# Optimization experiments

Hardware: AMD Instinct MI355X
Metric: run time of the kernel (lower is better)

## Reference

```python
import jax, jax.numpy as jnp
import numpy as np
from jax import lax

SEQ_LEN, N_FEAT, N_EMB, N_ENC, BATCH = 100, 18, 16, 16, 16384


def lstm(x, W_ih, W_hh, b_ih, b_hh, hidden):
    """PyTorch-convention LSTM (gates i,f,g,o), batch_first x: [B,T,I].
    Returns (h_seq [B,T,H], h_last [B,H])."""
    B = x.shape[0]
    # Precompute input projections for all timesteps: [B,T,4H]
    xg = jnp.einsum('bti,gi->btg', x, W_ih) + b_ih + b_hh
    W_hh_T = W_hh.T  # [H,4H]

    def step(carry, xg_t):
        h, c = carry
        g = xg_t + h @ W_hh_T                       # [B,4H]
        i, f, gg, o = jnp.split(g, 4, axis=-1)
        i = jax.nn.sigmoid(i)
        f = jax.nn.sigmoid(f)
        gg = jnp.tanh(gg)
        o = jax.nn.sigmoid(o)
        c = f * c + i * gg
        h = o * jnp.tanh(c)
        return (h, c), h

    h0 = jnp.zeros((B, hidden), x.dtype)
    c0 = jnp.zeros((B, hidden), x.dtype)
    (h_last, _), h_seq = lax.scan(step, (h0, c0), jnp.swapaxes(xg, 0, 1))
    return jnp.swapaxes(h_seq, 0, 1), h_last


def setup_inputs() -> dict:
    key = jax.random.key(0)
    ks = jax.random.split(key, 9)
    s1 = 1.0 / np.sqrt(N_EMB)
    s2 = 1.0 / np.sqrt(N_ENC)
    u = lambda k, shape, s: jax.random.uniform(k, shape, jnp.float32, -s, s)
    return {
        'x': jax.random.normal(ks[0], (BATCH, SEQ_LEN, N_FEAT), jnp.float32),
        'W_ih1': u(ks[1], (4 * N_EMB, N_FEAT), s1),
        'W_hh1': u(ks[2], (4 * N_EMB, N_EMB), s1),
        'b_ih1': u(ks[3], (4 * N_EMB,), s1),
        'b_hh1': u(ks[4], (4 * N_EMB,), s1),
        'W_ih2': u(ks[5], (4 * N_ENC, N_EMB), s2),
        'W_hh2': u(ks[6], (4 * N_ENC, N_ENC), s2),
        'b_ih2': u(ks[7], (4 * N_ENC,), s2),
        'b_hh2': u(ks[8], (4 * N_ENC,), s2),
    }


def reference(x, W_ih1, W_hh1, b_ih1, b_hh1, W_ih2, W_hh2, b_ih2, b_hh2):
    h1_seq, _ = lstm(x, W_ih1, W_hh1, b_ih1, b_hh1, N_EMB)
    h1_seq = jax.nn.relu(h1_seq)
    _, h2_last = lstm(h1_seq, W_ih2, W_hh2, b_ih2, b_hh2, N_ENC)
    return jax.nn.relu(h2_last)  # [B, N_ENC]
```

## Files before the change

### kernel.cpp

```cpp
#include <hip/hip_runtime.h>


typedef float f32x4 __attribute__((ext_vector_type(4)));
typedef __bf16 bf16x8 __attribute__((ext_vector_type(8)));
typedef unsigned int uint32x4 __attribute__((ext_vector_type(4)));

union FragU { bf16x8 v; unsigned short u[8]; unsigned int d[4]; uint32x4 q; };

#define MFMA16(A, B, C) __builtin_amdgcn_mfma_f32_16x16x32_bf16((A), (B), (C), 0, 0, 0)

static __device__ __forceinline__ unsigned short f2bf(float f) {
  unsigned int u = __builtin_bit_cast(unsigned int, f);
  u = u + 0x7FFFu + ((u >> 16) & 1u);
  return (unsigned short)(u >> 16);
}
static __device__ __forceinline__ float bfbits2f(unsigned short h) {
  unsigned int u = ((unsigned int)h) << 16;
  return __builtin_bit_cast(float, u);
}
static __device__ __forceinline__ float sigm(float x) {
  return __builtin_amdgcn_rcpf(1.0f + __builtin_amdgcn_exp2f(x * -1.4426950408889634f));
}
static __device__ __forceinline__ float tanh_(float x) {
  return 1.0f - 2.0f * __builtin_amdgcn_rcpf(1.0f + __builtin_amdgcn_exp2f(x * 2.8853900817779268f));
}
static __device__ __forceinline__ unsigned int split_pack(float v) {
  unsigned int u = __builtin_bit_cast(unsigned int, v);
  float hf = __builtin_bit_cast(float, u & 0xFFFF0000u);
  unsigned int l = __builtin_bit_cast(unsigned int, v - hf);
  return (u >> 16) | (l & 0xFFFF0000u);
}
static __device__ __forceinline__ void cvt_pair(float f0, float f1,
                                                unsigned int& hd, unsigned int& ld) {
  unsigned int u0 = __builtin_bit_cast(unsigned int, f0);
  unsigned int u1 = __builtin_bit_cast(unsigned int, f1);
  unsigned int h0 = u0 & 0xFFFF0000u;
  unsigned int h1 = u1 & 0xFFFF0000u;
  hd = (u0 >> 16) | h1;
  unsigned int l0 = __builtin_bit_cast(unsigned int, f0 - __builtin_bit_cast(float, h0));
  unsigned int l1 = __builtin_bit_cast(unsigned int, f1 - __builtin_bit_cast(float, h1));
  ld = (l0 >> 16) | (l1 & 0xFFFF0000u);
}

struct RawX { float2 a, b2, c, d; };

__global__ __launch_bounds__(256, 1) void enc_kernel(
    const float* __restrict__ x,
    const float* __restrict__ Wih1,
    const float* __restrict__ Whh1,
    const float* __restrict__ bih1,
    const float* __restrict__ bhh1,
    const float* __restrict__ Wih2,
    const float* __restrict__ Whh2,
    const float* __restrict__ bih2,
    const float* __restrict__ bhh2,
    float* __restrict__ out)
{
  const int lane = threadIdx.x & 63;
  const int b    = lane & 15;
  const int g    = lane >> 4;

  const int wid = (int)((blockIdx.x * blockDim.x + threadIdx.x) >> 6);
  const int b0  = wid * 16;

  FragU A1h[4], A1l[4], A2h[4], A2l[4], A3h[4], A3l[4], A4h[4], A4l[4];
  f32x4 bias1v[4], bias2v[4];
#pragma unroll
  for (int tn = 0; tn < 4; ++tn) {
    const int row = tn * 16 + b;
#pragma unroll
    for (int j = 0; j < 8; ++j) {
      const int k = 8 * g + j;
      if (k < 18) {
        const float w = Wih1[row * 18 + k];
        A1h[tn].u[j] = f2bf(w);
        A1l[tn].u[j] = f2bf(w - bfbits2f(A1h[tn].u[j]));
      } else {
        A1h[tn].u[j] = 0;
        A1l[tn].u[j] = 0;
      }
      const int kk = k >> 1;
      const float w2 = Whh1[row * 16 + kk];
      const float w3 = Wih2[row * 16 + kk];
      const float w4 = Whh2[row * 16 + kk];
      A2h[tn].u[j] = f2bf(w2); A2l[tn].u[j] = f2bf(w2 - bfbits2f(A2h[tn].u[j]));
      A3h[tn].u[j] = f2bf(w3); A3l[tn].u[j] = f2bf(w3 - bfbits2f(A3h[tn].u[j]));
      A4h[tn].u[j] = f2bf(w4); A4l[tn].u[j] = f2bf(w4 - bfbits2f(A4h[tn].u[j]));
    }
#pragma unroll
    for (int r = 0; r < 4; ++r) {
      const int u4 = tn * 16 + 4 * g + r;
      bias1v[tn][r] = bih1[u4] + bhh1[u4];
      bias2v[tn][r] = bih2[u4] + bhh2[u4];
    }
  }

  const float* const x0 = x + (size_t)(b0 + b) * 1800 + 8 * g;
  const int adv = (g == 3) ? 0 : 18;

  auto loadraw = [&](const float* p) -> RawX {
    RawX r;
    r.a = *(const float2*)p;
    if (g < 2) {
      r.b2 = *(const float2*)(p + 2);
      r.c  = *(const float2*)(p + 4);
      r.d  = *(const float2*)(p + 6);
    } else {
      r.b2 = r.c = r.d = make_float2(0.f, 0.f);
    }
    return r;
  };
  auto cvt = [&](const RawX& rw, FragU& hi, FragU& lo) {
    cvt_pair(rw.a.x, rw.a.y, hi.d[0], lo.d[0]);
    cvt_pair(rw.b2.x, rw.b2.y, hi.d[1], lo.d[1]);
    cvt_pair(rw.c.x, rw.c.y, hi.d[2], lo.d[2]);
    cvt_pair(rw.d.x, rw.d.y, hi.d[3], lo.d[3]);
  };

  RawX rw0 = loadraw(x0);
  RawX rw1 = loadraw(x0 + adv);
  RawX rw  = loadraw(x0 + 2 * adv);
  const float* xq = x0 + 3 * adv;

  FragU hb, h2b;
  hb.q  = (uint32x4){0u, 0u, 0u, 0u};
  h2b.q = (uint32x4){0u, 0u, 0u, 0u};
  float c1[4] = {0.f, 0.f, 0.f, 0.f};
  float c2[4] = {0.f, 0.f, 0.f, 0.f};
  float h2v[4] = {0.f, 0.f, 0.f, 0.f};

  FragU xch, xcl;
  cvt(rw0, xch, xcl);

  f32x4 ga[4];
#pragma unroll
  for (int tn = 0; tn < 4; ++tn) {
    f32x4 acc = MFMA16(A1h[tn].v, xch.v, bias1v[tn]);
    acc = MFMA16(A1l[tn].v, xch.v, acc);
    acc = MFMA16(A1h[tn].v, xcl.v, acc);
    acc = MFMA16(A2h[tn].v, hb.v, acc);
    acc = MFMA16(A2l[tn].v, hb.v, acc);
    ga[tn] = acc;
  }
  cvt(rw1, xch, xcl);

#pragma unroll 2
  for (int t = 0; t < 100; ++t) {
    FragU rb;
#pragma unroll
    for (int r = 0; r < 4; ++r) {
      const float iv = sigm(ga[0][r]);
      const float fv = sigm(ga[1][r]);
      const float gv = tanh_(ga[2][r]);
      const float ov = sigm(ga[3][r]);
      const float cc = fv * c1[r] + iv * gv;
      c1[r] = cc;
      const float h = ov * tanh_(cc);
      const unsigned int pk = split_pack(h);
      hb.d[r] = pk;
      rb.d[r] = (h > 0.f) ? pk : 0u;
    }

    f32x4 gb[4];
#pragma unroll
    for (int tn = 0; tn < 4; ++tn) {
      f32x4 acc = MFMA16(A4h[tn].v, h2b.v, bias2v[tn]);
      acc = MFMA16(A4l[tn].v, h2b.v, acc);
      acc = MFMA16(A3h[tn].v, rb.v, acc);
      acc = MFMA16(A3l[tn].v, rb.v, acc);
      gb[tn] = acc;
    }

    f32x4 gan[4];
#pragma unroll
    for (int tn = 0; tn < 4; ++tn) {
      f32x4 acc = MFMA16(A1h[tn].v, xch.v, bias1v[tn]);
      acc = MFMA16(A1l[tn].v, xch.v, acc);
      acc = MFMA16(A1h[tn].v, xcl.v, acc);
      acc = MFMA16(A2h[tn].v, hb.v, acc);
      acc = MFMA16(A2l[tn].v, hb.v, acc);
      gan[tn] = acc;
    }

    FragU nxh, nxl;
    cvt(rw, nxh, nxl);

    RawX rwn = loadraw((t <= 96) ? xq : x0);
    xq += adv;

#pragma unroll
    for (int r = 0; r < 4; ++r) {
      const float iv = sigm(gb[0][r]);
      const float fv = sigm(gb[1][r]);
      const float gv = tanh_(gb[2][r]);
      const float ov = sigm(gb[3][r]);
      const float cc = fv * c2[r] + iv * gv;
      c2[r] = cc;
      const float h = ov * tanh_(cc);
      h2v[r] = h;
      h2b.d[r] = split_pack(h);
    }

#pragma unroll
    for (int tn = 0; tn < 4; ++tn) ga[tn] = gan[tn];
    xch = nxh;
    xcl = nxl;
    rw = rwn;
  }

  f32x4 o;
#pragma unroll
  for (int r = 0; r < 4; ++r) o[r] = fmaxf(h2v[r], 0.f);
  *(f32x4*)(out + (size_t)(b0 + b) * 16 + 4 * g) = o;

  (void)x0;
}

extern "C" void kernel_launch(void* const* d_in, const int* in_sizes, int n_in,
                              void* d_out, int out_size, void* d_ws, size_t ws_size,
                              hipStream_t stream) {
  (void)in_sizes; (void)n_in; (void)d_ws; (void)ws_size; (void)out_size;
  enc_kernel<<<dim3(256), dim3(256), 0, stream>>>(
      (const float*)d_in[0],
      (const float*)d_in[1],
      (const float*)d_in[2],
      (const float*)d_in[3],
      (const float*)d_in[4],
      (const float*)d_in[5],
      (const float*)d_in[6],
      (const float*)d_in[7],
      (const float*)d_in[8],
      (float*)d_out);
}
```

Baseline: 270.3 us.

## Split the two LSTM layers into producer and consumer wavefronts linked through LDS

```diff
diff --git a/kernel.cpp b/kernel.cpp
--- a/kernel.cpp
+++ b/kernel.cpp
@@ -42,9 +42,14 @@
   ld = (l0 >> 16) | (l1 & 0xFFFF0000u);
 }
 
+static __device__ __forceinline__ void wg_barrier() {
+  asm volatile("s_waitcnt lgkmcnt(0)" ::: "memory");
+  __builtin_amdgcn_s_barrier();
+}
+
 struct RawX { float2 a, b2, c, d; };
 
-__global__ __launch_bounds__(256, 1) void enc_kernel(
+__global__ __launch_bounds__(128, 2) void enc_kernel(
     const float* __restrict__ x,
     const float* __restrict__ Wih1,
     const float* __restrict__ Whh1,
@@ -60,118 +65,74 @@
   const int b    = lane & 15;
   const int g    = lane >> 4;
 
-  const int wid = (int)((blockIdx.x * blockDim.x + threadIdx.x) >> 6);
-  const int b0  = wid * 16;
-
-  FragU A1h[4], A1l[4], A2h[4], A2l[4], A3h[4], A3l[4], A4h[4], A4l[4];
-  f32x4 bias1v[4], bias2v[4];
-#pragma unroll
-  for (int tn = 0; tn < 4; ++tn) {
-    const int row = tn * 16 + b;
-#pragma unroll
-    for (int j = 0; j < 8; ++j) {
-      const int k = 8 * g + j;
-      if (k < 18) {
-        const float w = Wih1[row * 18 + k];
-        A1h[tn].u[j] = f2bf(w);
-        A1l[tn].u[j] = f2bf(w - bfbits2f(A1h[tn].u[j]));
+  const int role = ((int)(threadIdx.x >> 6) ^ (int)blockIdx.x) & 1;
+  const int b0   = (int)blockIdx.x * 16;
+
+  __shared__ uint32x4 hxc[2][64];
+
+  if (role == 0) {
+    FragU A1h[4], A1l[4], A2h[4], A2l[4];
+    f32x4 bias1v[4];
+#pragma unroll
+    for (int tn = 0; tn < 4; ++tn) {
+      const int row = tn * 16 + b;
+#pragma unroll
+      for (int j = 0; j < 8; ++j) {
+        const int k = 8 * g + j;
+        if (k < 18) {
+          const float w = Wih1[row * 18 + k];
+          A1h[tn].u[j] = f2bf(w);
+          A1l[tn].u[j] = f2bf(w - bfbits2f(A1h[tn].u[j]));
+        } else {
+          A1h[tn].u[j] = 0;
+          A1l[tn].u[j] = 0;
+        }
+        const int kk = k >> 1;
+        const float w2 = Whh1[row * 16 + kk];
+        A2h[tn].u[j] = f2bf(w2); A2l[tn].u[j] = f2bf(w2 - bfbits2f(A2h[tn].u[j]));
+      }
+#pragma unroll
+      for (int r = 0; r < 4; ++r) {
+        const int u4 = tn * 16 + 4 * g + r;
+        bias1v[tn][r] = bih1[u4] + bhh1[u4];
+      }
+    }
+
+    const float* const x0 = x + (size_t)(b0 + b) * 1800 + 8 * g;
+    const int adv = (g == 3) ? 0 : 18;
+
+    auto loadraw = [&](const float* p) -> RawX {
+      RawX r;
+      r.a = *(const float2*)p;
+      if (g < 2) {
+        r.b2 = *(const float2*)(p + 2);
+        r.c  = *(const float2*)(p + 4);
+        r.d  = *(const float2*)(p + 6);
       } else {
-        A1h[tn].u[j] = 0;
-        A1l[tn].u[j] = 0;
-      }
-      const int kk = k >> 1;
-      const float w2 = Whh1[row * 16 + kk];
-      const float w3 = Wih2[row * 16 + kk];
-      const float w4 = Whh2[row * 16 + kk];
-      A2h[tn].u[j] = f2bf(w2); A2l[tn].u[j] = f2bf(w2 - bfbits2f(A2h[tn].u[j]));
-      A3h[tn].u[j] = f2bf(w3); A3l[tn].u[j] = f2bf(w3 - bfbits2f(A3h[tn].u[j]));
-      A4h[tn].u[j] = f2bf(w4); A4l[tn].u[j] = f2bf(w4 - bfbits2f(A4h[tn].u[j]));
-    }
-#pragma unroll
-    for (int r = 0; r < 4; ++r) {
-      const int u4 = tn * 16 + 4 * g + r;
-      bias1v[tn][r] = bih1[u4] + bhh1[u4];
-      bias2v[tn][r] = bih2[u4] + bhh2[u4];
-    }
-  }
-
-  const float* const x0 = x + (size_t)(b0 + b) * 1800 + 8 * g;
-  const int adv = (g == 3) ? 0 : 18;
-
-  auto loadraw = [&](const float* p) -> RawX {
-    RawX r;
-    r.a = *(const float2*)p;
-    if (g < 2) {
-      r.b2 = *(const float2*)(p + 2);
-      r.c  = *(const float2*)(p + 4);
-      r.d  = *(const float2*)(p + 6);
-    } else {
-      r.b2 = r.c = r.d = make_float2(0.f, 0.f);
-    }
-    return r;
-  };
-  auto cvt = [&](const RawX& rw, FragU& hi, FragU& lo) {
-    cvt_pair(rw.a.x, rw.a.y, hi.d[0], lo.d[0]);
-    cvt_pair(rw.b2.x, rw.b2.y, hi.d[1], lo.d[1]);
-    cvt_pair(rw.c.x, rw.c.y, hi.d[2], lo.d[2]);
-    cvt_pair(rw.d.x, rw.d.y, hi.d[3], lo.d[3]);
-  };
-
-  RawX rw0 = loadraw(x0);
-  RawX rw1 = loadraw(x0 + adv);
-  RawX rw  = loadraw(x0 + 2 * adv);
-  const float* xq = x0 + 3 * adv;
-
-  FragU hb, h2b;
-  hb.q  = (uint32x4){0u, 0u, 0u, 0u};
-  h2b.q = (uint32x4){0u, 0u, 0u, 0u};
-  float c1[4] = {0.f, 0.f, 0.f, 0.f};
-  float c2[4] = {0.f, 0.f, 0.f, 0.f};
-  float h2v[4] = {0.f, 0.f, 0.f, 0.f};
-
-  FragU xch, xcl;
-  cvt(rw0, xch, xcl);
-
-  f32x4 ga[4];
-#pragma unroll
-  for (int tn = 0; tn < 4; ++tn) {
-    f32x4 acc = MFMA16(A1h[tn].v, xch.v, bias1v[tn]);
-    acc = MFMA16(A1l[tn].v, xch.v, acc);
-    acc = MFMA16(A1h[tn].v, xcl.v, acc);
-    acc = MFMA16(A2h[tn].v, hb.v, acc);
-    acc = MFMA16(A2l[tn].v, hb.v, acc);
-    ga[tn] = acc;
-  }
-  cvt(rw1, xch, xcl);
-
-#pragma unroll 2
-  for (int t = 0; t < 100; ++t) {
-    FragU rb;
-#pragma unroll
-    for (int r = 0; r < 4; ++r) {
-      const float iv = sigm(ga[0][r]);
-      const float fv = sigm(ga[1][r]);
-      const float gv = tanh_(ga[2][r]);
-      const float ov = sigm(ga[3][r]);
-      const float cc = fv * c1[r] + iv * gv;
-      c1[r] = cc;
-      const float h = ov * tanh_(cc);
-      const unsigned int pk = split_pack(h);
-      hb.d[r] = pk;
-      rb.d[r] = (h > 0.f) ? pk : 0u;
-    }
-
-    f32x4 gb[4];
-#pragma unroll
-    for (int tn = 0; tn < 4; ++tn) {
-      f32x4 acc = MFMA16(A4h[tn].v, h2b.v, bias2v[tn]);
-      acc = MFMA16(A4l[tn].v, h2b.v, acc);
-      acc = MFMA16(A3h[tn].v, rb.v, acc);
-      acc = MFMA16(A3l[tn].v, rb.v, acc);
-      gb[tn] = acc;
-    }
-
-    f32x4 gan[4];
+        r.b2 = r.c = r.d = make_float2(0.f, 0.f);
+      }
+      return r;
+    };
+    auto cvt = [&](const RawX& rw_, FragU& hi, FragU& lo) {
+      cvt_pair(rw_.a.x, rw_.a.y, hi.d[0], lo.d[0]);
+      cvt_pair(rw_.b2.x, rw_.b2.y, hi.d[1], lo.d[1]);
+      cvt_pair(rw_.c.x, rw_.c.y, hi.d[2], lo.d[2]);
+      cvt_pair(rw_.d.x, rw_.d.y, hi.d[3], lo.d[3]);
+    };
+
+    RawX rw0 = loadraw(x0);
+    RawX rw1 = loadraw(x0 + adv);
+    RawX rw  = loadraw(x0 + 2 * adv);
+    const float* xq = x0 + 3 * adv;
+
+    FragU hb;
+    hb.q = (uint32x4){0u, 0u, 0u, 0u};
+    float c1[4] = {0.f, 0.f, 0.f, 0.f};
+
+    FragU xch, xcl;
+    cvt(rw0, xch, xcl);
+
+    f32x4 ga[4];
 #pragma unroll
     for (int tn = 0; tn < 4; ++tn) {
       f32x4 acc = MFMA16(A1h[tn].v, xch.v, bias1v[tn]);
@@ -179,48 +140,121 @@
       acc = MFMA16(A1h[tn].v, xcl.v, acc);
       acc = MFMA16(A2h[tn].v, hb.v, acc);
       acc = MFMA16(A2l[tn].v, hb.v, acc);
-      gan[tn] = acc;
-    }
-
-    FragU nxh, nxl;
-    cvt(rw, nxh, nxl);
-
-    RawX rwn = loadraw((t <= 96) ? xq : x0);
-    xq += adv;
-
-#pragma unroll
-    for (int r = 0; r < 4; ++r) {
-      const float iv = sigm(gb[0][r]);
-      const float fv = sigm(gb[1][r]);
-      const float gv = tanh_(gb[2][r]);
-      const float ov = sigm(gb[3][r]);
-      const float cc = fv * c2[r] + iv * gv;
-      c2[r] = cc;
-      const float h = ov * tanh_(cc);
-      h2v[r] = h;
-      h2b.d[r] = split_pack(h);
-    }
-
-#pragma unroll
-    for (int tn = 0; tn < 4; ++tn) ga[tn] = gan[tn];
-    xch = nxh;
-    xcl = nxl;
-    rw = rwn;
+      ga[tn] = acc;
+    }
+    cvt(rw1, xch, xcl);
+
+#pragma unroll 2
+    for (int t = 0; t < 100; ++t) {
+      FragU rb;
+#pragma unroll
+      for (int r = 0; r < 4; ++r) {
+        const float iv = sigm(ga[0][r]);
+        const float fv = sigm(ga[1][r]);
+        const float gv = tanh_(ga[2][r]);
+        const float ov = sigm(ga[3][r]);
+        const float cc = fv * c1[r] + iv * gv;
+        c1[r] = cc;
+        const float h = ov * tanh_(cc);
+        const unsigned int pk = split_pack(h);
+        hb.d[r] = pk;
+        rb.d[r] = (h > 0.f) ? pk : 0u;
+      }
+      hxc[t & 1][lane] = rb.q;
+
+      f32x4 gan[4];
+#pragma unroll
+      for (int tn = 0; tn < 4; ++tn) {
+        f32x4 acc = MFMA16(A1h[tn].v, xch.v, bias1v[tn]);
+        acc = MFMA16(A1l[tn].v, xch.v, acc);
+        acc = MFMA16(A1h[tn].v, xcl.v, acc);
+        acc = MFMA16(A2h[tn].v, hb.v, acc);
+        acc = MFMA16(A2l[tn].v, hb.v, acc);
+        gan[tn] = acc;
+      }
+
+      FragU nxh, nxl;
+      cvt(rw, nxh, nxl);
+      RawX rwn = loadraw((t <= 96) ? xq : x0);
+      xq += adv;
+
+#pragma unroll
+      for (int tn = 0; tn < 4; ++tn) ga[tn] = gan[tn];
+      xch = nxh;
+      xcl = nxl;
+      rw = rwn;
+
+      wg_barrier();
+    }
+  } else {
+    FragU A3h[4], A3l[4], A4h[4], A4l[4];
+    f32x4 bias2v[4];
+#pragma unroll
+    for (int tn = 0; tn < 4; ++tn) {
+      const int row = tn * 16 + b;
+#pragma unroll
+      for (int j = 0; j < 8; ++j) {
+        const int kk = (8 * g + j) >> 1;
+        const float w3 = Wih2[row * 16 + kk];
+        const float w4 = Whh2[row * 16 + kk];
+        A3h[tn].u[j] = f2bf(w3); A3l[tn].u[j] = f2bf(w3 - bfbits2f(A3h[tn].u[j]));
+        A4h[tn].u[j] = f2bf(w4); A4l[tn].u[j] = f2bf(w4 - bfbits2f(A4h[tn].u[j]));
+      }
+#pragma unroll
+      for (int r = 0; r < 4; ++r) {
+        const int u4 = tn * 16 + 4 * g + r;
+        bias2v[tn][r] = bih2[u4] + bhh2[u4];
+      }
+    }
+
+    FragU h2b;
+    h2b.q = (uint32x4){0u, 0u, 0u, 0u};
+    float c2[4] = {0.f, 0.f, 0.f, 0.f};
+    float h2v[4] = {0.f, 0.f, 0.f, 0.f};
+
+#pragma unroll 2
+    for (int t = 0; t < 100; ++t) {
+      wg_barrier();
+
+      FragU rbp;
+      rbp.q = hxc[t & 1][lane];
+
+      f32x4 gb[4];
+#pragma unroll
+      for (int tn = 0; tn < 4; ++tn) {
+        f32x4 acc = MFMA16(A4h[tn].v, h2b.v, bias2v[tn]);
+        acc = MFMA16(A4l[tn].v, h2b.v, acc);
+        acc = MFMA16(A3h[tn].v, rbp.v, acc);
+        acc = MFMA16(A3l[tn].v, rbp.v, acc);
+        gb[tn] = acc;
+      }
+
+#pragma unroll
+      for (int r = 0; r < 4; ++r) {
+        const float iv = sigm(gb[0][r]);
+        const float fv = sigm(gb[1][r]);
+        const float gv = tanh_(gb[2][r]);
+        const float ov = sigm(gb[3][r]);
+        const float cc = fv * c2[r] + iv * gv;
+        c2[r] = cc;
+        const float h = ov * tanh_(cc);
+        h2v[r] = h;
+        h2b.d[r] = split_pack(h);
+      }
+    }
+
+    f32x4 o;
+#pragma unroll
+    for (int r = 0; r < 4; ++r) o[r] = fmaxf(h2v[r], 0.f);
+    *(f32x4*)(out + (size_t)(b0 + b) * 16 + 4 * g) = o;
   }
-
-  f32x4 o;
-#pragma unroll
-  for (int r = 0; r < 4; ++r) o[r] = fmaxf(h2v[r], 0.f);
-  *(f32x4*)(out + (size_t)(b0 + b) * 16 + 4 * g) = o;
-
-  (void)x0;
 }
 
 extern "C" void kernel_launch(void* const* d_in, const int* in_sizes, int n_in,
                               void* d_out, int out_size, void* d_ws, size_t ws_size,
                               hipStream_t stream) {
   (void)in_sizes; (void)n_in; (void)d_ws; (void)ws_size; (void)out_size;
-  enc_kernel<<<dim3(256), dim3(256), 0, stream>>>(
+  enc_kernel<<<dim3(1024), dim3(128), 0, stream>>>(
       (const float*)d_in[0],
       (const float*)d_in[1],
       (const float*)d_in[2],
```

Result: no change. 275.2 us (+1.8%).

## Split input-projection MFMAs off the recurrent chain and use v_perm packing

Applied to the files above, without the earlier changes.

```diff
diff --git a/kernel.cpp b/kernel.cpp
--- a/kernel.cpp
+++ b/kernel.cpp
@@ -28,7 +28,7 @@
   unsigned int u = __builtin_bit_cast(unsigned int, v);
   float hf = __builtin_bit_cast(float, u & 0xFFFF0000u);
   unsigned int l = __builtin_bit_cast(unsigned int, v - hf);
-  return (u >> 16) | (l & 0xFFFF0000u);
+  return __builtin_amdgcn_perm(l, u, 0x07060302u);
 }
 static __device__ __forceinline__ void cvt_pair(float f0, float f1,
                                                 unsigned int& hd, unsigned int& ld) {
@@ -36,10 +36,10 @@
   unsigned int u1 = __builtin_bit_cast(unsigned int, f1);
   unsigned int h0 = u0 & 0xFFFF0000u;
   unsigned int h1 = u1 & 0xFFFF0000u;
-  hd = (u0 >> 16) | h1;
+  hd = __builtin_amdgcn_perm(u1, u0, 0x07060302u);
   unsigned int l0 = __builtin_bit_cast(unsigned int, f0 - __builtin_bit_cast(float, h0));
   unsigned int l1 = __builtin_bit_cast(unsigned int, f1 - __builtin_bit_cast(float, h1));
-  ld = (l0 >> 16) | (l1 & 0xFFFF0000u);
+  ld = __builtin_amdgcn_perm(l1, l0, 0x07060302u);
 }
 
 struct RawX { float2 a, b2, c, d; };
@@ -95,6 +95,8 @@
     }
   }
 
+  const f32x4 z4 = {0.f, 0.f, 0.f, 0.f};
+
   const float* const x0 = x + (size_t)(b0 + b) * 1800 + 8 * g;
   const int adv = (g == 3) ? 0 : 18;
 
@@ -110,11 +112,11 @@
     }
     return r;
   };
-  auto cvt = [&](const RawX& rw, FragU& hi, FragU& lo) {
-    cvt_pair(rw.a.x, rw.a.y, hi.d[0], lo.d[0]);
-    cvt_pair(rw.b2.x, rw.b2.y, hi.d[1], lo.d[1]);
-    cvt_pair(rw.c.x, rw.c.y, hi.d[2], lo.d[2]);
-    cvt_pair(rw.d.x, rw.d.y, hi.d[3], lo.d[3]);
+  auto cvt = [&](const RawX& rw_, FragU& hi, FragU& lo) {
+    cvt_pair(rw_.a.x, rw_.a.y, hi.d[0], lo.d[0]);
+    cvt_pair(rw_.b2.x, rw_.b2.y, hi.d[1], lo.d[1]);
+    cvt_pair(rw_.c.x, rw_.c.y, hi.d[2], lo.d[2]);
+    cvt_pair(rw_.d.x, rw_.d.y, hi.d[3], lo.d[3]);
   };
 
   RawX rw0 = loadraw(x0);
@@ -138,14 +140,28 @@
     f32x4 acc = MFMA16(A1h[tn].v, xch.v, bias1v[tn]);
     acc = MFMA16(A1l[tn].v, xch.v, acc);
     acc = MFMA16(A1h[tn].v, xcl.v, acc);
-    acc = MFMA16(A2h[tn].v, hb.v, acc);
-    acc = MFMA16(A2l[tn].v, hb.v, acc);
     ga[tn] = acc;
   }
   cvt(rw1, xch, xcl);
 
 #pragma unroll 2
   for (int t = 0; t < 100; ++t) {
+    f32x4 gx[4];
+#pragma unroll
+    for (int tn = 0; tn < 4; ++tn) {
+      f32x4 acc = MFMA16(A1h[tn].v, xch.v, bias1v[tn]);
+      acc = MFMA16(A1l[tn].v, xch.v, acc);
+      acc = MFMA16(A1h[tn].v, xcl.v, acc);
+      gx[tn] = acc;
+    }
+    f32x4 q2[4];
+#pragma unroll
+    for (int tn = 0; tn < 4; ++tn) {
+      f32x4 acc = MFMA16(A4h[tn].v, h2b.v, bias2v[tn]);
+      acc = MFMA16(A4l[tn].v, h2b.v, acc);
+      q2[tn] = acc;
+    }
+
     FragU rb;
 #pragma unroll
     for (int r = 0; r < 4; ++r) {
@@ -164,22 +180,17 @@
     f32x4 gb[4];
 #pragma unroll
     for (int tn = 0; tn < 4; ++tn) {
-      f32x4 acc = MFMA16(A4h[tn].v, h2b.v, bias2v[tn]);
-      acc = MFMA16(A4l[tn].v, h2b.v, acc);
-      acc = MFMA16(A3h[tn].v, rb.v, acc);
+      f32x4 acc = MFMA16(A3h[tn].v, rb.v, z4);
       acc = MFMA16(A3l[tn].v, rb.v, acc);
-      gb[tn] = acc;
+      gb[tn] = q2[tn] + acc;
     }
 
     f32x4 gan[4];
 #pragma unroll
     for (int tn = 0; tn < 4; ++tn) {
-      f32x4 acc = MFMA16(A1h[tn].v, xch.v, bias1v[tn]);
-      acc = MFMA16(A1l[tn].v, xch.v, acc);
-      acc = MFMA16(A1h[tn].v, xcl.v, acc);
-      acc = MFMA16(A2h[tn].v, hb.v, acc);
+      f32x4 acc = MFMA16(A2h[tn].v, hb.v, z4);
       acc = MFMA16(A2l[tn].v, hb.v, acc);
-      gan[tn] = acc;
+      gan[tn] = gx[tn] + acc;
     }
 
     FragU nxh, nxl;
```

After: 305.0 us. 12.8% more time.

## Halve batch per wavefront and split gate math across lane halves

Applied to the files above, without the earlier changes.

```diff
diff --git a/kernel.cpp b/kernel.cpp
--- a/kernel.cpp
+++ b/kernel.cpp
@@ -28,7 +28,7 @@
   unsigned int u = __builtin_bit_cast(unsigned int, v);
   float hf = __builtin_bit_cast(float, u & 0xFFFF0000u);
   unsigned int l = __builtin_bit_cast(unsigned int, v - hf);
-  return (u >> 16) | (l & 0xFFFF0000u);
+  return __builtin_amdgcn_perm(l, u, 0x07060302u);
 }
 static __device__ __forceinline__ void cvt_pair(float f0, float f1,
                                                 unsigned int& hd, unsigned int& ld) {
@@ -36,15 +36,15 @@
   unsigned int u1 = __builtin_bit_cast(unsigned int, f1);
   unsigned int h0 = u0 & 0xFFFF0000u;
   unsigned int h1 = u1 & 0xFFFF0000u;
-  hd = (u0 >> 16) | h1;
+  hd = __builtin_amdgcn_perm(u1, u0, 0x07060302u);
   unsigned int l0 = __builtin_bit_cast(unsigned int, f0 - __builtin_bit_cast(float, h0));
   unsigned int l1 = __builtin_bit_cast(unsigned int, f1 - __builtin_bit_cast(float, h1));
-  ld = (l0 >> 16) | (l1 & 0xFFFF0000u);
+  ld = __builtin_amdgcn_perm(l1, l0, 0x07060302u);
 }
 
 struct RawX { float2 a, b2, c, d; };
 
-__global__ __launch_bounds__(256, 1) void enc_kernel(
+__global__ __launch_bounds__(256, 2) void enc_kernel(
     const float* __restrict__ x,
     const float* __restrict__ Wih1,
     const float* __restrict__ Whh1,
@@ -59,9 +59,10 @@
   const int lane = threadIdx.x & 63;
   const int b    = lane & 15;
   const int g    = lane >> 4;
+  const bool lo  = (b < 8);
 
   const int wid = (int)((blockIdx.x * blockDim.x + threadIdx.x) >> 6);
-  const int b0  = wid * 16;
+  const int b0  = wid * 8;
 
   FragU A1h[4], A1l[4], A2h[4], A2l[4], A3h[4], A3l[4], A4h[4], A4l[4];
   f32x4 bias1v[4], bias2v[4];
@@ -95,7 +96,7 @@
     }
   }
 
-  const float* const x0 = x + (size_t)(b0 + b) * 1800 + 8 * g;
+  const float* const x0 = x + (size_t)(b0 + (b & 7)) * 1800 + 8 * g;
   const int adv = (g == 3) ? 0 : 18;
 
   auto loadraw = [&](const float* p) -> RawX {
@@ -110,11 +111,11 @@
     }
     return r;
   };
-  auto cvt = [&](const RawX& rw, FragU& hi, FragU& lo) {
-    cvt_pair(rw.a.x, rw.a.y, hi.d[0], lo.d[0]);
-    cvt_pair(rw.b2.x, rw.b2.y, hi.d[1], lo.d[1]);
-    cvt_pair(rw.c.x, rw.c.y, hi.d[2], lo.d[2]);
-    cvt_pair(rw.d.x, rw.d.y, hi.d[3], lo.d[3]);
+  auto cvt = [&](const RawX& rw_, FragU& hi, FragU& lo_) {
+    cvt_pair(rw_.a.x, rw_.a.y, hi.d[0], lo_.d[0]);
+    cvt_pair(rw_.b2.x, rw_.b2.y, hi.d[1], lo_.d[1]);
+    cvt_pair(rw_.c.x, rw_.c.y, hi.d[2], lo_.d[2]);
+    cvt_pair(rw_.d.x, rw_.d.y, hi.d[3], lo_.d[3]);
   };
 
   RawX rw0 = loadraw(x0);
@@ -125,9 +126,9 @@
   FragU hb, h2b;
   hb.q  = (uint32x4){0u, 0u, 0u, 0u};
   h2b.q = (uint32x4){0u, 0u, 0u, 0u};
-  float c1[4] = {0.f, 0.f, 0.f, 0.f};
-  float c2[4] = {0.f, 0.f, 0.f, 0.f};
-  float h2v[4] = {0.f, 0.f, 0.f, 0.f};
+  float c1s0 = 0.f, c1s1 = 0.f;
+  float c2s0 = 0.f, c2s1 = 0.f;
+  float h2o0 = 0.f, h2o1 = 0.f;
 
   FragU xch, xcl;
   cvt(rw0, xch, xcl);
@@ -146,72 +147,94 @@
 
 #pragma unroll 2
   for (int t = 0; t < 100; ++t) {
-    FragU rb;
-#pragma unroll
-    for (int r = 0; r < 4; ++r) {
-      const float iv = sigm(ga[0][r]);
-      const float fv = sigm(ga[1][r]);
-      const float gv = tanh_(ga[2][r]);
-      const float ov = sigm(ga[3][r]);
-      const float cc = fv * c1[r] + iv * gv;
-      c1[r] = cc;
-      const float h = ov * tanh_(cc);
-      const unsigned int pk = split_pack(h);
-      hb.d[r] = pk;
-      rb.d[r] = (h > 0.f) ? pk : 0u;
-    }
-
-    f32x4 gb[4];
-#pragma unroll
-    for (int tn = 0; tn < 4; ++tn) {
-      f32x4 acc = MFMA16(A4h[tn].v, h2b.v, bias2v[tn]);
-      acc = MFMA16(A4l[tn].v, h2b.v, acc);
-      acc = MFMA16(A3h[tn].v, rb.v, acc);
-      acc = MFMA16(A3l[tn].v, rb.v, acc);
-      gb[tn] = acc;
-    }
-
-    f32x4 gan[4];
-#pragma unroll
-    for (int tn = 0; tn < 4; ++tn) {
-      f32x4 acc = MFMA16(A1h[tn].v, xch.v, bias1v[tn]);
-      acc = MFMA16(A1l[tn].v, xch.v, acc);
-      acc = MFMA16(A1h[tn].v, xcl.v, acc);
-      acc = MFMA16(A2h[tn].v, hb.v, acc);
-      acc = MFMA16(A2l[tn].v, hb.v, acc);
-      gan[tn] = acc;
-    }
-
-    FragU nxh, nxl;
-    cvt(rw, nxh, nxl);
-
-    RawX rwn = loadraw((t <= 96) ? xq : x0);
-    xq += adv;
-
-#pragma unroll
-    for (int r = 0; r < 4; ++r) {
-      const float iv = sigm(gb[0][r]);
-      const float fv = sigm(gb[1][r]);
-      const float gv = tanh_(gb[2][r]);
-      const float ov = sigm(gb[3][r]);
-      const float cc = fv * c2[r] + iv * gv;
-      c2[r] = cc;
-      const float h = ov * tanh_(cc);
-      h2v[r] = h;
-      h2b.d[r] = split_pack(h);
-    }
-
-#pragma unroll
-    for (int tn = 0; tn < 4; ++tn) ga[tn] = gan[tn];
-    xch = nxh;
-    xcl = nxl;
-    rw = rwn;
+    {
+      const float pi0 = lo ? ga[0][0] : ga[0][2];
+      const float pi1 = lo ? ga[0][1] : ga[0][3];
+      const float pf0 = lo ? ga[1][0] : ga[1][2];
+      const float pf1 = lo ? ga[1][1] : ga[1][3];
+      const float pg0 = lo ? ga[2][0] : ga[2][2];
+      const float pg1 = lo ? ga[2][1] : ga[2][3];
+      const float po0 = lo ? ga[3][0] : ga[3][2];
+      const float po1 = lo ? ga[3][1] : ga[3][3];
+      const float cc0 = sigm(pf0) * c1s0 + sigm(pi0) * tanh_(pg0);
+      const float cc1 = sigm(pf1) * c1s1 + sigm(pi1) * tanh_(pg1);
+      c1s0 = cc0; c1s1 = cc1;
+      const float h0 = sigm(po0) * tanh_(cc0);
+      const float h1 = sigm(po1) * tanh_(cc1);
+      const unsigned int pk0 = split_pack(h0);
+      const unsigned int pk1 = split_pack(h1);
+      const unsigned int rk0 = (h0 > 0.f) ? pk0 : 0u;
+      const unsigned int rk1 = (h1 > 0.f) ? pk1 : 0u;
+      const unsigned int qp0 = (unsigned int)__shfl_xor((int)pk0, 8, 64);
+      const unsigned int qp1 = (unsigned int)__shfl_xor((int)pk1, 8, 64);
+      const unsigned int qr0 = (unsigned int)__shfl_xor((int)rk0, 8, 64);
+      const unsigned int qr1 = (unsigned int)__shfl_xor((int)rk1, 8, 64);
+      hb.d[0] = lo ? pk0 : qp0;  hb.d[1] = lo ? pk1 : qp1;
+      hb.d[2] = lo ? qp0 : pk0;  hb.d[3] = lo ? qp1 : pk1;
+      FragU rb;
+      rb.d[0] = lo ? rk0 : qr0;  rb.d[1] = lo ? rk1 : qr1;
+      rb.d[2] = lo ? qr0 : rk0;  rb.d[3] = lo ? qr1 : rk1;
+
+      f32x4 gb[4];
+#pragma unroll
+      for (int tn = 0; tn < 4; ++tn) {
+        f32x4 acc = MFMA16(A4h[tn].v, h2b.v, bias2v[tn]);
+        acc = MFMA16(A4l[tn].v, h2b.v, acc);
+        acc = MFMA16(A3h[tn].v, rb.v, acc);
+        acc = MFMA16(A3l[tn].v, rb.v, acc);
+        gb[tn] = acc;
+      }
+
+      f32x4 gan[4];
+#pragma unroll
+      for (int tn = 0; tn < 4; ++tn) {
+        f32x4 acc = MFMA16(A1h[tn].v, xch.v, bias1v[tn]);
+        acc = MFMA16(A1l[tn].v, xch.v, acc);
+        acc = MFMA16(A1h[tn].v, xcl.v, acc);
+        acc = MFMA16(A2h[tn].v, hb.v, acc);
+        acc = MFMA16(A2l[tn].v, hb.v, acc);
+        gan[tn] = acc;
+      }
+
+      FragU nxh, nxl;
+      cvt(rw, nxh, nxl);
+
+      RawX rwn = loadraw((t <= 96) ? xq : x0);
+      xq += adv;
+
+      const float qi0 = lo ? gb[0][0] : gb[0][2];
+      const float qi1 = lo ? gb[0][1] : gb[0][3];
+      const float qf0 = lo ? gb[1][0] : gb[1][2];
+      const float qf1 = lo ? gb[1][1] : gb[1][3];
+      const float qg0 = lo ? gb[2][0] : gb[2][2];
+      const float qg1 = lo ? gb[2][1] : gb[2][3];
+      const float qo0 = lo ? gb[3][0] : gb[3][2];
+      const float qo1 = lo ? gb[3][1] : gb[3][3];
+      const float dd0 = sigm(qf0) * c2s0 + sigm(qi0) * tanh_(qg0);
+      const float dd1 = sigm(qf1) * c2s1 + sigm(qi1) * tanh_(qg1);
+      c2s0 = dd0; c2s1 = dd1;
+      const float g0 = sigm(qo0) * tanh_(dd0);
+      const float g1 = sigm(qo1) * tanh_(dd1);
+      h2o0 = g0; h2o1 = g1;
+      const unsigned int hk0 = split_pack(g0);
+      const unsigned int hk1 = split_pack(g1);
+      const unsigned int qh0 = (unsigned int)__shfl_xor((int)hk0, 8, 64);
+      const unsigned int qh1 = (unsigned int)__shfl_xor((int)hk1, 8, 64);
+      h2b.d[0] = lo ? hk0 : qh0;  h2b.d[1] = lo ? hk1 : qh1;
+      h2b.d[2] = lo ? qh0 : hk0;  h2b.d[3] = lo ? qh1 : hk1;
+
+#pragma unroll
+      for (int tn = 0; tn < 4; ++tn) ga[tn] = gan[tn];
+      xch = nxh;
+      xcl = nxl;
+      rw = rwn;
+    }
   }
 
-  f32x4 o;
-#pragma unroll
-  for (int r = 0; r < 4; ++r) o[r] = fmaxf(h2v[r], 0.f);
-  *(f32x4*)(out + (size_t)(b0 + b) * 16 + 4 * g) = o;
+  float2 o;
+  o.x = fmaxf(h2o0, 0.f);
+  o.y = fmaxf(h2o1, 0.f);
+  *(float2*)(out + (size_t)(b0 + (b & 7)) * 16 + 4 * g + (lo ? 0 : 2)) = o;
 
   (void)x0;
 }
@@ -220,7 +243,7 @@
                               void* d_out, int out_size, void* d_ws, size_t ws_size,
                               hipStream_t stream) {
   (void)in_sizes; (void)n_in; (void)d_ws; (void)ws_size; (void)out_size;
-  enc_kernel<<<dim3(256), dim3(256), 0, stream>>>(
+  enc_kernel<<<dim3(512), dim3(256), 0, stream>>>(
       (const float*)d_in[0],
       (const float*)d_in[1],
       (const float*)d_in[2],
```

New measurement: 301.5 us. 11.5% more time.
